# Kernel optimization log

Hardware: AMD Instinct MI355X
Metric: run time of the kernel (lower is better)

## Reference

```python
import jax, jax.numpy as jnp
import numpy as np

C = 256          # channels
G = 16           # dcn groups
K = 3            # dcn kernel size (P = K*K sampling points)
PAD = 1
DIL = 1
OFFSET_SCALE = 1.0
HIDDEN = 4 * C   # mlp_ratio = 4
EPS = 1e-6


def layer_norm(x, g, b):
    mu = x.mean(-1, keepdims=True)
    var = jnp.mean((x - mu) ** 2, -1, keepdims=True)
    return (x - mu) * jax.lax.rsqrt(var + EPS) * g + b


def grid_sample_bilinear(img, grid):
    """img: (B,Cg,H,W); grid: (B,L,P,2) xy in [-1,1].
    Matches F.grid_sample(mode='bilinear', padding_mode='zeros', align_corners=False)."""
    B, Cg, H, W = img.shape
    x = (grid[..., 0] + 1.0) * (W * 0.5) - 0.5
    y = (grid[..., 1] + 1.0) * (H * 0.5) - 0.5
    x0f = jnp.floor(x); y0f = jnp.floor(y)
    wx1 = x - x0f; wy1 = y - y0f
    x0 = x0f.astype(jnp.int32); y0 = y0f.astype(jnp.int32)
    flat = img.reshape(B, Cg, H * W)

    def tap(ix, iy, w):
        valid = (ix >= 0) & (ix < W) & (iy >= 0) & (iy < H)
        idx = jnp.clip(iy, 0, H - 1) * W + jnp.clip(ix, 0, W - 1)
        v = jnp.take_along_axis(flat, idx.reshape(B, 1, -1), axis=2)
        v = v.reshape(B, Cg, idx.shape[1], idx.shape[2])
        return v * (w * valid)[:, None]

    return (tap(x0, y0, (1 - wx1) * (1 - wy1))
            + tap(x0 + 1, y0, wx1 * (1 - wy1))
            + tap(x0, y0 + 1, (1 - wx1) * wy1)
            + tap(x0 + 1, y0 + 1, wx1 * wy1))


def dcnv3(x, dw_w, dw_b, off_w, off_b, mask_w, mask_b, inp_w, inp_b, out_w, out_b):
    """DCNv3 forward (dcnv3_core_pytorch math), x: (N,H,W,C) channels_last."""
    N, H, W, Cc = x.shape
    Cg = Cc // G
    P = K * K
    xp = x @ inp_w.T + inp_b                             # input_proj
    x1 = jax.lax.conv_general_dilated(
        x, dw_w, (1, 1), [(PAD, PAD), (PAD, PAD)],
        dimension_numbers=('NHWC', 'HWIO', 'NHWC'),
        feature_group_count=Cc) + dw_b                   # depthwise conv
    off = (x1 @ off_w.T + off_b).reshape(N, H, W, G, P, 2)
    m = jax.nn.softmax((x1 @ mask_w.T + mask_b).reshape(N, H, W, G, P), axis=-1)
    Hin, Win = H + 2 * PAD, W + 2 * PAD
    xpad = jnp.pad(xp, ((0, 0), (PAD, PAD), (PAD, PAD), (0, 0)))
    base = (DIL * (K - 1)) // 2
    ry = (jnp.arange(H, dtype=x.dtype) * 1.0 + base + 0.5) / Hin
    rx = (jnp.arange(W, dtype=x.dtype) * 1.0 + base + 0.5) / Win
    ref = jnp.stack([jnp.broadcast_to(rx[None, :], (H, W)),
                     jnp.broadcast_to(ry[:, None], (H, W))], -1)   # (H,W,2) xy
    xs = (jnp.arange(K, dtype=x.dtype) * DIL - base) / Win
    ys = (jnp.arange(K, dtype=x.dtype) * DIL - base) / Hin
    gx, gy = jnp.meshgrid(xs, ys, indexing='ij')         # w-major order as in torch ref
    grid = jnp.stack([gx, gy], -1).reshape(P, 2)
    norm = jnp.array([Win, Hin], dtype=x.dtype)
    loc = (ref[None, :, :, None, None, :] + grid * OFFSET_SCALE
           + off * (OFFSET_SCALE / norm))                # (N,H,W,G,P,2)
    sg = 2.0 * loc - 1.0
    img = xpad.reshape(N, Hin, Win, G, Cg).transpose(0, 3, 4, 1, 2).reshape(N * G, Cg, Hin, Win)
    sgr = sg.transpose(0, 3, 1, 2, 4, 5).reshape(N * G, H * W, P, 2)
    sampled = grid_sample_bilinear(img, sgr)             # (N*G,Cg,HW,P)
    mr = m.transpose(0, 3, 1, 2, 4).reshape(N * G, 1, H * W, P)
    out = (sampled * mr).sum(-1).reshape(N, G, Cg, H * W)
    out = out.transpose(0, 3, 1, 2).reshape(N, H, W, Cc)
    return out @ out_w.T + out_b                         # output_proj


def setup_inputs() -> dict:
    key = jax.random.key(0)
    ks = jax.random.split(key, 10)
    N, H, W = 8, 56, 56
    P = K * K

    def rn(k, shape, s):
        return jax.random.normal(k, shape, dtype=jnp.float32) * s

    return {
        'x': jax.random.normal(ks[0], (N, H, W, C), dtype=jnp.float32),
        'ln1_g': jnp.ones((C,), jnp.float32), 'ln1_b': jnp.zeros((C,), jnp.float32),
        'dw_w': rn(ks[1], (K, K, 1, C), 0.1), 'dw_b': jnp.zeros((C,), jnp.float32),
        'off_w': rn(ks[2], (G * P * 2, C), 0.02), 'off_b': jnp.zeros((G * P * 2,), jnp.float32),
        'mask_w': rn(ks[3], (G * P, C), 0.02), 'mask_b': jnp.zeros((G * P,), jnp.float32),
        'inp_w': rn(ks[4], (C, C), 0.05), 'inp_b': jnp.zeros((C,), jnp.float32),
        'out_w': rn(ks[5], (C, C), 0.05), 'out_b': jnp.zeros((C,), jnp.float32),
        'ln2_g': jnp.ones((C,), jnp.float32), 'ln2_b': jnp.zeros((C,), jnp.float32),
        'fc1_w': rn(ks[6], (HIDDEN, C), 0.05), 'fc1_b': jnp.zeros((HIDDEN,), jnp.float32),
        'fc2_w': rn(ks[7], (C, HIDDEN), 0.05), 'fc2_b': jnp.zeros((C,), jnp.float32),
    }


def reference(x, ln1_g, ln1_b, dw_w, dw_b, off_w, off_b, mask_w, mask_b,
              inp_w, inp_b, out_w, out_b, ln2_g, ln2_b, fc1_w, fc1_b, fc2_w, fc2_b):
    # pre-norm block, no layer_scale, drop_path=0
    y = x + dcnv3(layer_norm(x, ln1_g, ln1_b), dw_w, dw_b, off_w, off_b,
                  mask_w, mask_b, inp_w, inp_b, out_w, out_b)
    h = layer_norm(y, ln2_g, ln2_b)
    h = jax.nn.gelu(h @ fc1_w.T + fc1_b, approximate=False)
    return y + (h @ fc2_w.T + fc2_b)
```

## Files before the change

kernel.cpp:

```cpp
#include <hip/hip_runtime.h>
#include <hip/hip_bf16.h>
#include <math.h>

#define NTOK 25088
#define HW_  3136
#define HH   56
#define WW   56
#define CCH  256
#define NGRP 16
#define NPTS 9
#define HIDN 1024
#define NOFFM 432
#define TPB  8

typedef __attribute__((ext_vector_type(8))) __bf16 bf16x8;
typedef __attribute__((ext_vector_type(4))) __bf16 bf16x4;
typedef __attribute__((ext_vector_type(4))) float  f32x4;
typedef __attribute__((ext_vector_type(4))) _Float16 f16x4;
typedef __attribute__((ext_vector_type(8))) _Float16 f16x8;

static __device__ __forceinline__ void gl_lds16(const void* g, void* l) {
    __builtin_amdgcn_global_load_lds((const __attribute__((address_space(1))) void*)g,
                                     (__attribute__((address_space(3))) void*)l, 16, 0, 0);
}

static __device__ __forceinline__ f16x8 splat8(_Float16 w) {
    f16x8 r = {w, w, w, w, w, w, w, w};
    return r;
}

static __device__ __forceinline__ float gelu_fast(float v) {
    float v2 = v * v;
    float z2 = fmaf(0.0713548163f * v, v2, 1.5957691216f * v);
    float r  = __builtin_amdgcn_rcpf(__expf(-z2) + 1.0f);
    return v * r;
}

__global__ __launch_bounds__(256)
void cvt_all_kernel(const float* __restrict__ inp_w, const float* __restrict__ out_w,
                    const float* __restrict__ off_w, const float* __restrict__ mask_w,
                    const float* __restrict__ fc1_w, const float* __restrict__ fc2_w,
                    const float* __restrict__ off_b, const float* __restrict__ mask_b,
                    __bf16* wib, __bf16* wob, __bf16* wcat, __bf16* w1b, __bf16* w2b,
                    float* bcat) {
    int i = blockIdx.x * 256 + threadIdx.x;
    if (i >= 191488) {
        int j = i - 191488;
        if (j < 432) bcat[j] = (j < 288) ? off_b[j] : mask_b[j - 288];
        return;
    }
    const float* s; __bf16* d; int off;
    if (i < 16384)       { s = inp_w;  d = wib;          off = i; }
    else if (i < 32768)  { s = out_w;  d = wob;          off = i - 16384; }
    else if (i < 51200)  { s = off_w;  d = wcat;         off = i - 32768; }
    else if (i < 60416)  { s = mask_w; d = wcat + 73728; off = i - 51200; }
    else if (i < 125952) { s = fc1_w;  d = w1b;          off = i - 60416; }
    else                 { s = fc2_w;  d = w2b;          off = i - 125952; }
    float4 v = ((const float4*)s)[off];
    bf16x4 o = {(__bf16)v.x, (__bf16)v.y, (__bf16)v.z, (__bf16)v.w};
    ((bf16x4*)d)[off] = o;
}

__global__ __launch_bounds__(256)
void ln_f_kernel(const float* __restrict__ x, const float* __restrict__ g,
                 const float* __restrict__ b, __bf16* __restrict__ outb) {
    int gid  = blockIdx.x * 256 + threadIdx.x;
    int t    = gid >> 6;
    int lane = threadIdx.x & 63;
    if (t >= NTOK) return;
    float4 v = ((const float4*)(x + (size_t)t * CCH))[lane];
    float s = v.x + v.y + v.z + v.w;
#pragma unroll
    for (int o = 1; o < 64; o <<= 1) s += __shfl_xor(s, o);
    float mu = s * 0.00390625f;
    float dx = v.x - mu, dy = v.y - mu, dz = v.z - mu, dw = v.w - mu;
    float q = dx * dx + dy * dy + dz * dz + dw * dw;
#pragma unroll
    for (int o = 1; o < 64; o <<= 1) q += __shfl_xor(q, o);
    float rstd = rsqrtf(q * 0.00390625f + 1e-6f);
    float4 gg = ((const float4*)g)[lane];
    float4 bb = ((const float4*)b)[lane];
    bf16x4 ob = {(__bf16)(dx * rstd * gg.x + bb.x), (__bf16)(dy * rstd * gg.y + bb.y),
                 (__bf16)(dz * rstd * gg.z + bb.z), (__bf16)(dw * rstd * gg.w + bb.w)};
    ((bf16x4*)(outb + (size_t)t * CCH))[lane] = ob;
}

__global__ __launch_bounds__(256)
void ln_b_kernel(const __bf16* __restrict__ x, const float* __restrict__ g,
                 const float* __restrict__ b, __bf16* __restrict__ outb) {
    int gid  = blockIdx.x * 256 + threadIdx.x;
    int t    = gid >> 6;
    int lane = threadIdx.x & 63;
    if (t >= NTOK) return;
    bf16x4 vb = ((const bf16x4*)(x + (size_t)t * CCH))[lane];
    float vx = (float)vb[0], vy = (float)vb[1], vz = (float)vb[2], vw = (float)vb[3];
    float s = vx + vy + vz + vw;
#pragma unroll
    for (int o = 1; o < 64; o <<= 1) s += __shfl_xor(s, o);
    float mu = s * 0.00390625f;
    float dx = vx - mu, dy = vy - mu, dz = vz - mu, dw = vw - mu;
    float q = dx * dx + dy * dy + dz * dz + dw * dw;
#pragma unroll
    for (int o = 1; o < 64; o <<= 1) q += __shfl_xor(q, o);
    float rstd = rsqrtf(q * 0.00390625f + 1e-6f);
    float4 gg = ((const float4*)g)[lane];
    float4 bb = ((const float4*)b)[lane];
    bf16x4 ob = {(__bf16)(dx * rstd * gg.x + bb.x), (__bf16)(dy * rstd * gg.y + bb.y),
                 (__bf16)(dz * rstd * gg.z + bb.z), (__bf16)(dw * rstd * gg.w + bb.w)};
    ((bf16x4*)(outb + (size_t)t * CCH))[lane] = ob;
}

__global__ __launch_bounds__(256)
void dwconv_kernel(const __bf16* __restrict__ ln, const float* __restrict__ wt,
                   const float* __restrict__ bias, __bf16* __restrict__ out) {
    int gid = blockIdx.x * 256 + threadIdx.x;
    int t = gid >> 6;
    int cq = gid & 63;
    if (t >= NTOK) return;
    int n = t / HW_, hw = t % HW_;
    int h = hw / WW, w0 = hw % WW;
    float4 a = ((const float4*)bias)[cq];
    const bf16x4* l4 = (const bf16x4*)ln;
    const float4* w4 = (const float4*)wt;
#pragma unroll
    for (int ky = 0; ky < 3; ++ky) {
        int y = h + ky - 1;
        if (y < 0 || y >= HH) continue;
#pragma unroll
        for (int kx = 0; kx < 3; ++kx) {
            int x = w0 + kx - 1;
            if (x < 0 || x >= WW) continue;
            bf16x4 v = l4[(size_t)(n * HW_ + y * WW + x) * 64 + cq];
            float4 ww = w4[(ky * 3 + kx) * 64 + cq];
            a.x += (float)v[0] * ww.x; a.y += (float)v[1] * ww.y;
            a.z += (float)v[2] * ww.z; a.w += (float)v[3] * ww.w;
        }
    }
    bf16x4 ob = {(__bf16)a.x, (__bf16)a.y, (__bf16)a.z, (__bf16)a.w};
    ((bf16x4*)out)[(size_t)t * 64 + cq] = ob;
}

template <int EPI>
static __device__ __forceinline__ void gemm_body(
        const __bf16* __restrict__ A, const __bf16* __restrict__ W,
        const float* __restrict__ bias, const float* __restrict__ residf,
        const __bf16* __restrict__ residb, float* __restrict__ outf,
        __bf16* __restrict__ outb, const int Ndim, const int Kdim,
        const int NB, const int lin) {
    __shared__ __align__(16) __bf16 Alds[2][64 * 32];
    __shared__ __align__(16) __bf16 Blds[2][128 * 32];

    const int tid  = threadIdx.x;
    const int w    = tid >> 6;
    const int lane = tid & 63;
    const int m0 = (lin / NB) * 64;
    const int n0 = (lin % NB) * 128;
    const int wr = (w >> 1) * 32;
    const int wc = (w & 1) * 64;

    f32x4 acc[2][4];
#pragma unroll
    for (int i = 0; i < 2; ++i)
#pragma unroll
        for (int j = 0; j < 4; ++j) acc[i][j] = (f32x4){0.f, 0.f, 0.f, 0.f};

    const int pA   = tid;
    const int arow = pA >> 2, abyte = ((pA & 3) ^ ((pA >> 4) & 3)) * 16;
    const int pB1  = tid + 256;
    const int br0  = tid >> 2, br1 = pB1 >> 2;
    int bR0 = n0 + ((br0 >> 6) << 6) + 4 * (br0 & 15) + ((br0 >> 4) & 3);
    int bR1 = n0 + ((br1 >> 6) << 6) + 4 * (br1 & 15) + ((br1 >> 4) & 3);
    if (bR0 > Ndim - 1) bR0 = Ndim - 1;
    if (bR1 > Ndim - 1) bR1 = Ndim - 1;
    const int bb0 = ((tid & 3) ^ ((tid >> 3) & 3)) * 16;
    const int bb1 = ((pB1 & 3) ^ ((pB1 >> 3) & 3)) * 16;

    const char* Ab = (const char*)A;
    const char* Wb = (const char*)W;
    char* AL = (char*)&Alds[0][0];
    char* BL = (char*)&Blds[0][0];
    const size_t rb  = (size_t)Kdim * 2;
    const size_t sA  = (size_t)(m0 + arow) * rb + abyte;
    const size_t sB0 = (size_t)bR0 * rb + bb0;
    const size_t sB1 = (size_t)bR1 * rb + bb1;
    const int dof = w * 1024;

#define STAGE(BUF, TILE)                                                        \
    do {                                                                        \
        const size_t kb_ = (size_t)(TILE) * 64;                                 \
        gl_lds16(Ab + sA  + kb_, AL + (BUF) * 4096 + dof);                      \
        gl_lds16(Wb + sB0 + kb_, BL + (BUF) * 8192 + dof);                      \
        gl_lds16(Wb + sB1 + kb_, BL + (BUF) * 8192 + 4096 + dof);               \
    } while (0)

    const int mrow = lane & 15;
    const int q    = lane >> 4;
    const int kA   = ((q ^ (mrow >> 2)) & 3) * 16;
    const int kB   = ((q ^ (mrow >> 1)) & 3) * 16;

    const int nt = Kdim >> 5;
    STAGE(0, 0);
    if (nt > 1) STAGE(1, 1);
    for (int i = 0; i < nt; ++i) {
        const int cur = i & 1;
        if (i + 1 < nt) asm volatile("s_waitcnt vmcnt(3)" ::: "memory");
        else            asm volatile("s_waitcnt vmcnt(0)" ::: "memory");
        __builtin_amdgcn_s_barrier();
        bf16x8 af[2], bfr[4];
#pragma unroll
        for (int ii = 0; ii < 2; ++ii)
            af[ii] = *(const bf16x8*)(AL + cur * 4096 + (wr + ii * 16 + mrow) * 64 + kA);
#pragma unroll
        for (int ii = 0; ii < 4; ++ii)
            bfr[ii] = *(const bf16x8*)(BL + cur * 8192 + (wc + ii * 16 + mrow) * 64 + kB);
#pragma unroll
        for (int mi = 0; mi < 2; ++mi)
#pragma unroll
            for (int ni = 0; ni < 4; ++ni)
                acc[mi][ni] = __builtin_amdgcn_mfma_f32_16x16x32_bf16(af[mi], bfr[ni], acc[mi][ni], 0, 0, 0);
        __builtin_amdgcn_s_barrier();
        if (i + 2 < nt) STAGE(cur, i + 2);
    }
#undef STAGE

    const int coll = lane & 15;
    const int rowh = (lane >> 4) * 4;
    const int col0 = n0 + wc + 4 * coll;
    if (col0 < Ndim) {
        const float4 bv = *(const float4*)(bias + col0);
#pragma unroll
        for (int mi = 0; mi < 2; ++mi) {
#pragma unroll
            for (int j = 0; j < 4; ++j) {
                const int row = m0 + wr + mi * 16 + rowh + j;
                const size_t idx = (size_t)row * (size_t)Ndim + col0;
                float4 v = make_float4(acc[mi][0][j] + bv.x, acc[mi][1][j] + bv.y,
                                       acc[mi][2][j] + bv.z, acc[mi][3][j] + bv.w);
                if (EPI == 2) {
                    bf16x4 ob = {(__bf16)gelu_fast(v.x), (__bf16)gelu_fast(v.y),
                                 (__bf16)gelu_fast(v.z), (__bf16)gelu_fast(v.w)};
                    *(bf16x4*)(outb + idx) = ob;
                } else if (EPI == 3) {
                    bf16x4 ob = {(__bf16)v.x, (__bf16)v.y, (__bf16)v.z, (__bf16)v.w};
                    *(bf16x4*)(outb + idx) = ob;
                } else if (EPI == 4) {
                    const float4 r = *(const float4*)(residf + idx);
                    bf16x4 ob = {(__bf16)(v.x + r.x), (__bf16)(v.y + r.y),
                                 (__bf16)(v.z + r.z), (__bf16)(v.w + r.w)};
                    *(bf16x4*)(outb + idx) = ob;
                } else if (EPI == 5) {
                    const bf16x4 r = *(const bf16x4*)(residb + idx);
                    v.x += (float)r[0]; v.y += (float)r[1];
                    v.z += (float)r[2]; v.w += (float)r[3];
                    *(float4*)(outf + idx) = v;
                } else {
                    f16x4 ob = {(_Float16)v.x, (_Float16)v.y, (_Float16)v.z, (_Float16)v.w};
                    *(f16x4*)((_Float16*)outb + idx) = ob;
                }
            }
        }
    }
}

template <int EPI>
__global__ __launch_bounds__(256, 6)
void gemm_kernel(const __bf16* __restrict__ A, const __bf16* __restrict__ W,
                 const float* __restrict__ bias, const float* __restrict__ residf,
                 const __bf16* __restrict__ residb, float* __restrict__ outf,
                 __bf16* __restrict__ outb, const int Ndim, const int Kdim, const int NB) {
    const int chunk = gridDim.x >> 3;
    const int lin   = (blockIdx.x & 7) * chunk + (blockIdx.x >> 3);
    gemm_body<EPI>(A, W, bias, residf, residb, outf, outb, Ndim, Kdim, NB, lin);
}

__global__ __launch_bounds__(256, 6)
void gemm_dual_kernel(const __bf16* __restrict__ A1, const __bf16* __restrict__ W1,
                      const float* __restrict__ b1, __bf16* __restrict__ o1,
                      const int N1, const int NB1, const int split,
                      const __bf16* __restrict__ A2, const __bf16* __restrict__ W2,
                      const float* __restrict__ b2, __bf16* __restrict__ o2,
                      const int N2, const int NB2) {
    const int chunk = gridDim.x >> 3;
    const int lin   = (blockIdx.x & 7) * chunk + (blockIdx.x >> 3);
    if (lin < split)
        gemm_body<3>(A1, W1, b1, nullptr, nullptr, nullptr, o1, N1, 256, NB1, lin);
    else
        gemm_body<6>(A2, W2, b2, nullptr, nullptr, nullptr, o2, N2, 256, NB2, lin - split);
}

__global__ __launch_bounds__(256)
void dcn_kernel(const _Float16* __restrict__ xp, const __bf16* __restrict__ om,
                __bf16* __restrict__ out) {
    __shared__ __align__(16) __bf16 rawb[TPB][NOFFM];
    __shared__ ushort4 sidx[NPTS][TPB * NGRP];
    __shared__ f16x4   swt[NPTS][TPB * NGRP];
    const int tid = threadIdx.x;
    const int bid = blockIdx.x;
    const int b   = (bid & 7) * 392 + (bid >> 3);
    const int t0  = b * TPB;

    for (int e = tid; e < (TPB * NOFFM) / 8; e += 256)
        *(bf16x8*)(&rawb[0][0] + e * 8) = *(const bf16x8*)(om + (size_t)t0 * NOFFM + e * 8);
    __syncthreads();

    if (tid < TPB * NGRP) {
        const int lt = tid >> 4, g = tid & 15;
        __bf16* m = &rawb[lt][288 + g * 9];
        float e[9];
        float mx = -1e30f;
#pragma unroll
        for (int p = 0; p < 9; ++p) { e[p] = (float)m[p]; mx = fmaxf(mx, e[p]); }
        float s = 0.f;
#pragma unroll
        for (int p = 0; p < 9; ++p) { e[p] = __expf(e[p] - mx); s += e[p]; }
        const float inv = 1.f / s;
#pragma unroll
        for (int p = 0; p < 9; ++p) m[p] = (__bf16)(e[p] * inv);
    }
    __syncthreads();

    for (int e = tid; e < TPB * NGRP * NPTS; e += 256) {
        const int lt = e / 144, r = e % 144, g = r / 9, p = r % 9;
        const int t  = t0 + lt;
        const int hw = t % HW_;
        const int h = hw / WW, w0 = hw % WW;
        const float offx = (float)rawb[lt][g * 18 + p * 2 + 0];
        const float offy = (float)rawb[lt][g * 18 + p * 2 + 1];
        const float pm   = (float)rawb[lt][288 + g * 9 + p];
        const int kx = p / 3, ky = p % 3;
        const float fx = (float)(w0 + kx - 1) + offx;
        const float fy = (float)(h  + ky - 1) + offy;
        const float x0f = floorf(fx), y0f = floorf(fy);
        const float wx = fx - x0f, wy = fy - y0f;
        const int x0 = (int)x0f, y0 = (int)y0f;
        const bool xv0 = (unsigned)x0 < WW, xv1 = (unsigned)(x0 + 1) < WW;
        const bool yv0 = (unsigned)y0 < HH, yv1 = (unsigned)(y0 + 1) < HH;
        const int xc0 = min(max(x0, 0), WW - 1), xc1 = min(max(x0 + 1, 0), WW - 1);
        const int yc0 = min(max(y0, 0), HH - 1), yc1 = min(max(y0 + 1, 0), HH - 1);
        const int tg = lt * 16 + g;
        sidx[p][tg] = make_ushort4((unsigned short)(yc0 * WW + xc0),
                                   (unsigned short)(yc0 * WW + xc1),
                                   (unsigned short)(yc1 * WW + xc0),
                                   (unsigned short)(yc1 * WW + xc1));
        f16x4 wv;
        wv[0] = (_Float16)((xv0 && yv0) ? (1.f - wx) * (1.f - wy) * pm : 0.f);
        wv[1] = (_Float16)((xv1 && yv0) ? wx * (1.f - wy) * pm : 0.f);
        wv[2] = (_Float16)((xv0 && yv1) ? (1.f - wx) * wy * pm : 0.f);
        wv[3] = (_Float16)((xv1 && yv1) ? wx * wy * pm : 0.f);
        swt[p][tg] = wv;
    }
    __syncthreads();

    const int lt = tid >> 5, lane = tid & 31;
    const int g = lane >> 1;
    const int t = t0 + lt;
    const int n = t / HW_;
    const int tg = lt * 16 + g;
    const _Float16* base = xp + (size_t)n * HW_ * CCH + lane * 8;
    f16x8 acc = {(_Float16)0, (_Float16)0, (_Float16)0, (_Float16)0,
                 (_Float16)0, (_Float16)0, (_Float16)0, (_Float16)0};
#pragma unroll
    for (int p = 0; p < NPTS; ++p) {
        const ushort4 id = sidx[p][tg];
        const f16x4   wh = swt[p][tg];
        f16x8 v0 = *(const f16x8*)(base + (size_t)id.x * CCH);
        f16x8 v1 = *(const f16x8*)(base + (size_t)id.y * CCH);
        f16x8 v2 = *(const f16x8*)(base + (size_t)id.z * CCH);
        f16x8 v3 = *(const f16x8*)(base + (size_t)id.w * CCH);
        acc += v0 * splat8(wh[0]) + v1 * splat8(wh[1])
             + v2 * splat8(wh[2]) + v3 * splat8(wh[3]);
    }
    bf16x8 ob;
#pragma unroll
    for (int k = 0; k < 8; ++k) ob[k] = (__bf16)(float)acc[k];
    *(bf16x8*)(out + (size_t)t * CCH + lane * 8) = ob;
}

extern "C" void kernel_launch(void* const* d_in, const int* in_sizes, int n_in,
                              void* d_out, int out_size, void* d_ws, size_t ws_size,
                              hipStream_t stream) {
    const float* x      = (const float*)d_in[0];
    const float* ln1_g  = (const float*)d_in[1];
    const float* ln1_b  = (const float*)d_in[2];
    const float* dw_w   = (const float*)d_in[3];
    const float* dw_b   = (const float*)d_in[4];
    const float* off_w  = (const float*)d_in[5];
    const float* off_b  = (const float*)d_in[6];
    const float* mask_w = (const float*)d_in[7];
    const float* mask_b = (const float*)d_in[8];
    const float* inp_w  = (const float*)d_in[9];
    const float* inp_b  = (const float*)d_in[10];
    const float* out_w  = (const float*)d_in[11];
    const float* out_b  = (const float*)d_in[12];
    const float* ln2_g  = (const float*)d_in[13];
    const float* ln2_b  = (const float*)d_in[14];
    const float* fc1_w  = (const float*)d_in[15];
    const float* fc1_b  = (const float*)d_in[16];
    const float* fc2_w  = (const float*)d_in[17];
    const float* fc2_b  = (const float*)d_in[18];
    float* out = (float*)d_out;

    char* ws = (char*)d_ws;
    size_t o = 0;
    auto alloc = [&](size_t bytes) { size_t r = o; o += (bytes + 255) & ~(size_t)255; return r; };
    __bf16* yb    = (__bf16*)(ws + alloc((size_t)NTOK * CCH * 2));
    __bf16* x1b   = (__bf16*)(ws + alloc((size_t)NTOK * CCH * 2));
    __bf16* lnb   = (__bf16*)(ws + alloc((size_t)NTOK * CCH * 2));
    __bf16* xpb   = (__bf16*)(ws + alloc((size_t)NTOK * CCH * 2));
    __bf16* offmb = (__bf16*)(ws + alloc((size_t)NTOK * NOFFM * 2));
    alloc(6 * 1024 * 1024);
    __bf16* wib   = (__bf16*)(ws + alloc((size_t)65536 * 2));
    __bf16* wob   = (__bf16*)(ws + alloc((size_t)65536 * 2));
    __bf16* wcat  = (__bf16*)(ws + alloc((size_t)110592 * 2));
    __bf16* w1b   = (__bf16*)(ws + alloc((size_t)262144 * 2));
    __bf16* w2b   = (__bf16*)(ws + alloc((size_t)262144 * 2));
    float*  bcat  = (float*)(ws + alloc((size_t)432 * 4));
    if (ws_size < o) return;

    __bf16* dcnb = lnb;
    __bf16* l2b  = x1b;
    __bf16* h1b  = lnb;

    cvt_all_kernel<<<750, 256, 0, stream>>>(inp_w, out_w, off_w, mask_w, fc1_w, fc2_w,
                                            off_b, mask_b, wib, wob, wcat, w1b, w2b, bcat);

    ln_f_kernel<<<NTOK / 4, 256, 0, stream>>>(x, ln1_g, ln1_b, lnb);
    dwconv_kernel<<<NTOK / 4, 256, 0, stream>>>(lnb, dw_w, dw_b, x1b);
    gemm_dual_kernel<<<392 * 4 + 392 * 2, 256, 0, stream>>>(
        x1b, wcat, bcat, offmb, NOFFM, 4, 392 * 4,
        lnb, wib, inp_b, xpb, 256, 2);
    dcn_kernel<<<NTOK / TPB, 256, 0, stream>>>((const _Float16*)xpb, offmb, dcnb);
    gemm_kernel<4><<<392 * 2, 256, 0, stream>>>(dcnb, wob, out_b, x, nullptr, nullptr, yb, 256, 256, 2);
    ln_b_kernel<<<NTOK / 4, 256, 0, stream>>>(yb, ln2_g, ln2_b, l2b);
    gemm_kernel<2><<<392 * 8, 256, 0, stream>>>(l2b, w1b, fc1_b, nullptr, nullptr, nullptr, h1b, 1024, 256, 8);
    gemm_kernel<5><<<392 * 2, 256, 0, stream>>>(h1b, w2b, fc2_b, nullptr, yb, out, nullptr, 256, 1024, 2);
}
```

Baseline: 160.2 us.

## Widen GEMM tiles to 64x256, fuse weight conversion with first layernorm

The GEMM body now computes a 64x256 output tile per block instead of 64x128. Each wave covers all 64 rows and a 64-column slice, so it holds a 4x4 grid of MFMA accumulators, and each block stages five 16-byte loads per tile. Grids are halved and the occupancy hint of 6 blocks per CU is dropped. This should improve operand reuse and cut the number of blocks, at the cost of more registers and LDS per block and fewer blocks for 25088 tokens. Separately, the weight-conversion kernel and the first layernorm are merged into one launch, and the DCN sampling loop's index decomposition is reordered to use shifts instead of divisions.

```diff
diff --git a/kernel.cpp b/kernel.cpp
--- a/kernel.cpp
+++ b/kernel.cpp
@@ -37,34 +37,34 @@
 }
 
 __global__ __launch_bounds__(256)
-void cvt_all_kernel(const float* __restrict__ inp_w, const float* __restrict__ out_w,
-                    const float* __restrict__ off_w, const float* __restrict__ mask_w,
-                    const float* __restrict__ fc1_w, const float* __restrict__ fc2_w,
-                    const float* __restrict__ off_b, const float* __restrict__ mask_b,
-                    __bf16* wib, __bf16* wob, __bf16* wcat, __bf16* w1b, __bf16* w2b,
-                    float* bcat) {
-    int i = blockIdx.x * 256 + threadIdx.x;
-    if (i >= 191488) {
-        int j = i - 191488;
-        if (j < 432) bcat[j] = (j < 288) ? off_b[j] : mask_b[j - 288];
+void cvtln_kernel(const float* __restrict__ inp_w, const float* __restrict__ out_w,
+                  const float* __restrict__ off_w, const float* __restrict__ mask_w,
+                  const float* __restrict__ fc1_w, const float* __restrict__ fc2_w,
+                  const float* __restrict__ off_b, const float* __restrict__ mask_b,
+                  __bf16* wib, __bf16* wob, __bf16* wcat, __bf16* w1b, __bf16* w2b,
+                  float* bcat,
+                  const float* __restrict__ x, const float* __restrict__ ln1_g,
+                  const float* __restrict__ ln1_b, __bf16* __restrict__ lnb) {
+    if (blockIdx.x < 750) {
+        int i = blockIdx.x * 256 + threadIdx.x;
+        if (i >= 191488) {
+            int j = i - 191488;
+            if (j < 432) bcat[j] = (j < 288) ? off_b[j] : mask_b[j - 288];
+            return;
+        }
+        const float* s; __bf16* d; int off;
+        if (i < 16384)       { s = inp_w;  d = wib;          off = i; }
+        else if (i < 32768)  { s = out_w;  d = wob;          off = i - 16384; }
+        else if (i < 51200)  { s = off_w;  d = wcat;         off = i - 32768; }
+        else if (i < 60416)  { s = mask_w; d = wcat + 73728; off = i - 51200; }
+        else if (i < 125952) { s = fc1_w;  d = w1b;          off = i - 60416; }
+        else                 { s = fc2_w;  d = w2b;          off = i - 125952; }
+        float4 v = ((const float4*)s)[off];
+        bf16x4 o = {(__bf16)v.x, (__bf16)v.y, (__bf16)v.z, (__bf16)v.w};
+        ((bf16x4*)d)[off] = o;
         return;
     }
-    const float* s; __bf16* d; int off;
-    if (i < 16384)       { s = inp_w;  d = wib;          off = i; }
-    else if (i < 32768)  { s = out_w;  d = wob;          off = i - 16384; }
-    else if (i < 51200)  { s = off_w;  d = wcat;         off = i - 32768; }
-    else if (i < 60416)  { s = mask_w; d = wcat + 73728; off = i - 51200; }
-    else if (i < 125952) { s = fc1_w;  d = w1b;          off = i - 60416; }
-    else                 { s = fc2_w;  d = w2b;          off = i - 125952; }
-    float4 v = ((const float4*)s)[off];
-    bf16x4 o = {(__bf16)v.x, (__bf16)v.y, (__bf16)v.z, (__bf16)v.w};
-    ((bf16x4*)d)[off] = o;
-}
-
-__global__ __launch_bounds__(256)
-void ln_f_kernel(const float* __restrict__ x, const float* __restrict__ g,
-                 const float* __restrict__ b, __bf16* __restrict__ outb) {
-    int gid  = blockIdx.x * 256 + threadIdx.x;
+    int gid  = (blockIdx.x - 750) * 256 + threadIdx.x;
     int t    = gid >> 6;
     int lane = threadIdx.x & 63;
     if (t >= NTOK) return;
@@ -78,11 +78,11 @@
 #pragma unroll
     for (int o = 1; o < 64; o <<= 1) q += __shfl_xor(q, o);
     float rstd = rsqrtf(q * 0.00390625f + 1e-6f);
-    float4 gg = ((const float4*)g)[lane];
-    float4 bb = ((const float4*)b)[lane];
+    float4 gg = ((const float4*)ln1_g)[lane];
+    float4 bb = ((const float4*)ln1_b)[lane];
     bf16x4 ob = {(__bf16)(dx * rstd * gg.x + bb.x), (__bf16)(dy * rstd * gg.y + bb.y),
                  (__bf16)(dz * rstd * gg.z + bb.z), (__bf16)(dw * rstd * gg.w + bb.w)};
-    ((bf16x4*)(outb + (size_t)t * CCH))[lane] = ob;
+    ((bf16x4*)(lnb + (size_t)t * CCH))[lane] = ob;
 }
 
 __global__ __launch_bounds__(256)
@@ -148,49 +148,58 @@
         __bf16* __restrict__ outb, const int Ndim, const int Kdim,
         const int NB, const int lin) {
     __shared__ __align__(16) __bf16 Alds[2][64 * 32];
-    __shared__ __align__(16) __bf16 Blds[2][128 * 32];
+    __shared__ __align__(16) __bf16 Blds[2][256 * 32];
 
     const int tid  = threadIdx.x;
     const int w    = tid >> 6;
     const int lane = tid & 63;
     const int m0 = (lin / NB) * 64;
-    const int n0 = (lin % NB) * 128;
-    const int wr = (w >> 1) * 32;
-    const int wc = (w & 1) * 64;
-
-    f32x4 acc[2][4];
-#pragma unroll
-    for (int i = 0; i < 2; ++i)
+    const int n0 = (lin % NB) * 256;
+    const int wc = w * 64;
+
+    f32x4 acc[4][4];
+#pragma unroll
+    for (int i = 0; i < 4; ++i)
 #pragma unroll
         for (int j = 0; j < 4; ++j) acc[i][j] = (f32x4){0.f, 0.f, 0.f, 0.f};
-
-    const int pA   = tid;
-    const int arow = pA >> 2, abyte = ((pA & 3) ^ ((pA >> 4) & 3)) * 16;
-    const int pB1  = tid + 256;
-    const int br0  = tid >> 2, br1 = pB1 >> 2;
-    int bR0 = n0 + ((br0 >> 6) << 6) + 4 * (br0 & 15) + ((br0 >> 4) & 3);
-    int bR1 = n0 + ((br1 >> 6) << 6) + 4 * (br1 & 15) + ((br1 >> 4) & 3);
-    if (bR0 > Ndim - 1) bR0 = Ndim - 1;
-    if (bR1 > Ndim - 1) bR1 = Ndim - 1;
-    const int bb0 = ((tid & 3) ^ ((tid >> 3) & 3)) * 16;
-    const int bb1 = ((pB1 & 3) ^ ((pB1 >> 3) & 3)) * 16;
 
     const char* Ab = (const char*)A;
     const char* Wb = (const char*)W;
     char* AL = (char*)&Alds[0][0];
     char* BL = (char*)&Blds[0][0];
-    const size_t rb  = (size_t)Kdim * 2;
-    const size_t sA  = (size_t)(m0 + arow) * rb + abyte;
-    const size_t sB0 = (size_t)bR0 * rb + bb0;
-    const size_t sB1 = (size_t)bR1 * rb + bb1;
-    const int dof = w * 1024;
-
-#define STAGE(BUF, TILE)                                                        \
-    do {                                                                        \
-        const size_t kb_ = (size_t)(TILE) * 64;                                 \
-        gl_lds16(Ab + sA  + kb_, AL + (BUF) * 4096 + dof);                      \
-        gl_lds16(Wb + sB0 + kb_, BL + (BUF) * 8192 + dof);                      \
-        gl_lds16(Wb + sB1 + kb_, BL + (BUF) * 8192 + 4096 + dof);               \
+    const size_t rb = (size_t)Kdim * 2;
+
+    const char* gsrc[5];
+    char*       ldst[5];
+    int         lstep[5];
+#pragma unroll
+    for (int k = 0; k < 5; ++k) {
+        const int sg = w * 5 + k;
+        if (sg < 4) {
+            const int p  = sg * 64 + lane;
+            const int rw = p >> 2;
+            const int ch = (p & 3) ^ ((p >> 4) & 3);
+            gsrc[k]  = Ab + (size_t)(m0 + rw) * rb + ch * 16;
+            ldst[k]  = AL + sg * 1024;
+            lstep[k] = 4096;
+        } else {
+            const int p  = (sg - 4) * 64 + lane;
+            const int r  = p >> 2;
+            int bR = n0 + ((r >> 6) << 6) + 4 * (r & 15) + ((r >> 4) & 3);
+            if (bR > Ndim - 1) bR = Ndim - 1;
+            const int ch = (p & 3) ^ ((p >> 3) & 3);
+            gsrc[k]  = Wb + (size_t)bR * rb + ch * 16;
+            ldst[k]  = BL + (sg - 4) * 1024;
+            lstep[k] = 16384;
+        }
+    }
+
+#define STAGE(BUF, TILE)                                              \
+    do {                                                              \
+        const size_t kb_ = (size_t)(TILE) * 64;                       \
+        _Pragma("unroll")                                             \
+        for (int k = 0; k < 5; ++k)                                   \
+            gl_lds16(gsrc[k] + kb_, ldst[k] + (BUF) * lstep[k]);      \
     } while (0)
 
     const int mrow = lane & 15;
@@ -203,18 +212,18 @@
     if (nt > 1) STAGE(1, 1);
     for (int i = 0; i < nt; ++i) {
         const int cur = i & 1;
-        if (i + 1 < nt) asm volatile("s_waitcnt vmcnt(3)" ::: "memory");
+        if (i + 1 < nt) asm volatile("s_waitcnt vmcnt(5)" ::: "memory");
         else            asm volatile("s_waitcnt vmcnt(0)" ::: "memory");
         __builtin_amdgcn_s_barrier();
-        bf16x8 af[2], bfr[4];
-#pragma unroll
-        for (int ii = 0; ii < 2; ++ii)
-            af[ii] = *(const bf16x8*)(AL + cur * 4096 + (wr + ii * 16 + mrow) * 64 + kA);
+        bf16x8 af[4], bfr[4];
 #pragma unroll
         for (int ii = 0; ii < 4; ++ii)
-            bfr[ii] = *(const bf16x8*)(BL + cur * 8192 + (wc + ii * 16 + mrow) * 64 + kB);
-#pragma unroll
-        for (int mi = 0; mi < 2; ++mi)
+            af[ii] = *(const bf16x8*)(AL + cur * 4096 + (ii * 16 + mrow) * 64 + kA);
+#pragma unroll
+        for (int ii = 0; ii < 4; ++ii)
+            bfr[ii] = *(const bf16x8*)(BL + cur * 16384 + (wc + ii * 16 + mrow) * 64 + kB);
+#pragma unroll
+        for (int mi = 0; mi < 4; ++mi)
 #pragma unroll
             for (int ni = 0; ni < 4; ++ni)
                 acc[mi][ni] = __builtin_amdgcn_mfma_f32_16x16x32_bf16(af[mi], bfr[ni], acc[mi][ni], 0, 0, 0);
@@ -224,15 +233,15 @@
 #undef STAGE
 
     const int coll = lane & 15;
-    const int rowh = (lane >> 4) * 4;
+    const int rowh = q * 4;
     const int col0 = n0 + wc + 4 * coll;
     if (col0 < Ndim) {
         const float4 bv = *(const float4*)(bias + col0);
 #pragma unroll
-        for (int mi = 0; mi < 2; ++mi) {
+        for (int mi = 0; mi < 4; ++mi) {
 #pragma unroll
             for (int j = 0; j < 4; ++j) {
-                const int row = m0 + wr + mi * 16 + rowh + j;
+                const int row = m0 + mi * 16 + rowh + j;
                 const size_t idx = (size_t)row * (size_t)Ndim + col0;
                 float4 v = make_float4(acc[mi][0][j] + bv.x, acc[mi][1][j] + bv.y,
                                        acc[mi][2][j] + bv.z, acc[mi][3][j] + bv.w);
@@ -263,7 +272,7 @@
 }
 
 template <int EPI>
-__global__ __launch_bounds__(256, 6)
+__global__ __launch_bounds__(256)
 void gemm_kernel(const __bf16* __restrict__ A, const __bf16* __restrict__ W,
                  const float* __restrict__ bias, const float* __restrict__ residf,
                  const __bf16* __restrict__ residb, float* __restrict__ outf,
@@ -273,7 +282,7 @@
     gemm_body<EPI>(A, W, bias, residf, residb, outf, outb, Ndim, Kdim, NB, lin);
 }
 
-__global__ __launch_bounds__(256, 6)
+__global__ __launch_bounds__(256)
 void gemm_dual_kernel(const __bf16* __restrict__ A1, const __bf16* __restrict__ W1,
                       const float* __restrict__ b1, __bf16* __restrict__ o1,
                       const int N1, const int NB1, const int split,
@@ -319,8 +328,10 @@
     }
     __syncthreads();
 
-    for (int e = tid; e < TPB * NGRP * NPTS; e += 256) {
-        const int lt = e / 144, r = e % 144, g = r / 9, p = r % 9;
+    for (int e = tid; e < NPTS * TPB * NGRP; e += 256) {
+        const int p  = e >> 7;
+        const int tg = e & 127;
+        const int lt = tg >> 4, g = tg & 15;
         const int t  = t0 + lt;
         const int hw = t % HW_;
         const int h = hw / WW, w0 = hw % WW;
@@ -337,7 +348,6 @@
         const bool yv0 = (unsigned)y0 < HH, yv1 = (unsigned)(y0 + 1) < HH;
         const int xc0 = min(max(x0, 0), WW - 1), xc1 = min(max(x0 + 1, 0), WW - 1);
         const int yc0 = min(max(y0, 0), HH - 1), yc1 = min(max(y0 + 1, 0), HH - 1);
-        const int tg = lt * 16 + g;
         sidx[p][tg] = make_ushort4((unsigned short)(yc0 * WW + xc0),
                                    (unsigned short)(yc0 * WW + xc1),
                                    (unsigned short)(yc1 * WW + xc0),
@@ -421,17 +431,17 @@
     __bf16* l2b  = x1b;
     __bf16* h1b  = lnb;
 
-    cvt_all_kernel<<<750, 256, 0, stream>>>(inp_w, out_w, off_w, mask_w, fc1_w, fc2_w,
-                                            off_b, mask_b, wib, wob, wcat, w1b, w2b, bcat);
-
-    ln_f_kernel<<<NTOK / 4, 256, 0, stream>>>(x, ln1_g, ln1_b, lnb);
+    cvtln_kernel<<<750 + NTOK / 4, 256, 0, stream>>>(
+        inp_w, out_w, off_w, mask_w, fc1_w, fc2_w, off_b, mask_b,
+        wib, wob, wcat, w1b, w2b, bcat, x, ln1_g, ln1_b, lnb);
+
     dwconv_kernel<<<NTOK / 4, 256, 0, stream>>>(lnb, dw_w, dw_b, x1b);
-    gemm_dual_kernel<<<392 * 4 + 392 * 2, 256, 0, stream>>>(
-        x1b, wcat, bcat, offmb, NOFFM, 4, 392 * 4,
-        lnb, wib, inp_b, xpb, 256, 2);
+    gemm_dual_kernel<<<392 * 2 + 392, 256, 0, stream>>>(
+        x1b, wcat, bcat, offmb, NOFFM, 2, 392 * 2,
+        lnb, wib, inp_b, xpb, 256, 1);
     dcn_kernel<<<NTOK / TPB, 256, 0, stream>>>((const _Float16*)xpb, offmb, dcnb);
-    gemm_kernel<4><<<392 * 2, 256, 0, stream>>>(dcnb, wob, out_b, x, nullptr, nullptr, yb, 256, 256, 2);
+    gemm_kernel<4><<<392, 256, 0, stream>>>(dcnb, wob, out_b, x, nullptr, nullptr, yb, 256, 256, 1);
     ln_b_kernel<<<NTOK / 4, 256, 0, stream>>>(yb, ln2_g, ln2_b, l2b);
-    gemm_kernel<2><<<392 * 8, 256, 0, stream>>>(l2b, w1b, fc1_b, nullptr, nullptr, nullptr, h1b, 1024, 256, 8);
-    gemm_kernel<5><<<392 * 2, 256, 0, stream>>>(h1b, w2b, fc2_b, nullptr, yb, out, nullptr, 256, 1024, 2);
-}
+    gemm_kernel<2><<<392 * 4, 256, 0, stream>>>(l2b, w1b, fc1_b, nullptr, nullptr, nullptr, h1b, 1024, 256, 4);
+    gemm_kernel<5><<<392, 256, 0, stream>>>(h1b, w2b, fc2_b, nullptr, yb, out, nullptr, 256, 1024, 1);
+}
```

Measured after the change: 159.9 us. No clear change (-0.2%).
